# Optimization experiments

Hardware: AMD Instinct MI355X
Metric: run time of the kernel (lower is better)

Reference implementation:

```python
import jax, jax.numpy as jnp
import numpy as np

F_DIM = 64
GRID_CYL = (512, 48)   # (grid0=azimuth, grid1=z)
CYL_RANGE = (-3.14159265, -2.0, 3.14159265, 4.0)
CYL_VS = ((CYL_RANGE[2] - CYL_RANGE[0]) / GRID_CYL[0], (CYL_RANGE[3] - CYL_RANGE[1]) / GRID_CYL[1])
PC_RANGE = (0.0, -40.0, -3.0, 70.4, 40.0, 1.0)
BEV_VS = (0.32, 0.32)
GRID_BEV = (220, 250)  # (grid0=x, grid1=y)
BEV_SCALE_XY = GRID_BEV[0] * GRID_BEV[1]
BEV_SCALE_Y = GRID_BEV[1]
CYL_SCALE_XY = GRID_CYL[0] * GRID_CYL[1]
CYL_SCALE_Y = GRID_CYL[1]
BN_EPS = 1e-3


def _bn_relu(x, g, b):
    # train-mode BatchNorm1d over point axis; x: [N, C]
    m = x.mean(0)
    v = jnp.mean((x - m) ** 2, 0)
    return jax.nn.relu((x - m) * jax.lax.rsqrt(v + BN_EPS) * g + b)


def setup_inputs():
    rng = np.random.default_rng(0)
    B, NP = 4, 50000
    N = B * NP
    bidx = np.repeat(np.arange(B), NP).astype(np.float32)
    x = rng.uniform(0.5, 70.0, N).astype(np.float32)
    y = rng.uniform(-39.9, 39.9, N).astype(np.float32)
    z = rng.uniform(-2.9, 0.9, N).astype(np.float32)
    inten = rng.uniform(0.0, 1.0, N).astype(np.float32)
    points = np.stack([bidx, x, y, z, inten], 1)
    rho = np.sqrt(x * x + y * y)
    phi = np.arctan2(y, x)
    points_cyl = np.stack([phi, z, rho], 1).astype(np.float32)
    cyl_idxs = np.stack([(phi - CYL_RANGE[0]) / CYL_VS[0], (z - CYL_RANGE[1]) / CYL_VS[1]], 1)
    cyl_idxs = np.minimum(np.maximum(cyl_idxs, 0.0), np.array(GRID_CYL) - 1e-3).astype(np.float32)
    bev_idxs = np.stack([(x - PC_RANGE[0]) / BEV_VS[0], (y - PC_RANGE[1]) / BEV_VS[1]], 1)
    bev_idxs = np.minimum(np.maximum(bev_idxs, 0.0), np.array(GRID_BEV) - 1e-3).astype(np.float32)
    bev_merge = bidx.astype(np.int64) * BEV_SCALE_XY + np.floor(bev_idxs[:, 0]).astype(np.int64) * BEV_SCALE_Y + np.floor(bev_idxs[:, 1]).astype(np.int64)
    bev_unq, bev_inv = np.unique(bev_merge, return_inverse=True)
    cyl_merge = bidx.astype(np.int64) * CYL_SCALE_XY + np.floor(cyl_idxs[:, 0]).astype(np.int64) * CYL_SCALE_Y + np.floor(cyl_idxs[:, 1]).astype(np.int64)
    cyl_unq, cyl_inv = np.unique(cyl_merge, return_inverse=True)

    def lin(o, i):
        return (rng.standard_normal((o, i)) / np.sqrt(i)).astype(np.float32)

    w1 = lin(F_DIM, 16)
    w2 = lin(2 * F_DIM, F_DIM)
    w3 = lin(F_DIM, 2 * F_DIM)
    wc = (rng.standard_normal((F_DIM, F_DIM, 3, 3)) / np.sqrt(F_DIM * 9)).astype(np.float32)

    def bn(c):
        return (1.0 + 0.1 * rng.standard_normal(c)).astype(np.float32), (0.1 * rng.standard_normal(c)).astype(np.float32)

    g1, b1 = bn(F_DIM)
    g2, b2 = bn(2 * F_DIM)
    gc, bc = bn(F_DIM)
    g3, b3 = bn(F_DIM)
    return {
        'points': jnp.asarray(points), 'points_cyl': jnp.asarray(points_cyl),
        'cyl_idxs': jnp.asarray(cyl_idxs), 'bev_idxs': jnp.asarray(bev_idxs),
        'w1': jnp.asarray(w1), 'g1': jnp.asarray(g1), 'b1': jnp.asarray(b1),
        'w2': jnp.asarray(w2), 'g2': jnp.asarray(g2), 'b2': jnp.asarray(b2),
        'wc': jnp.asarray(wc), 'gc': jnp.asarray(gc), 'bc': jnp.asarray(bc),
        'w3': jnp.asarray(w3), 'g3': jnp.asarray(g3), 'b3': jnp.asarray(b3),
        'bev_unq_inv': jnp.asarray(bev_inv.astype(np.int32)),
        'bev_unq_coords': jnp.asarray(bev_unq.astype(np.int32)),
        'cyl_unq_inv': jnp.asarray(cyl_inv.astype(np.int32)),
        'cyl_unq_coords': jnp.asarray(cyl_unq.astype(np.int32)),
        'batch_size': B,
    }


def reference(points, points_cyl, cyl_idxs, bev_idxs, w1, g1, b1, w2, g2, b2, wc, gc, bc, w3, g3, b3, bev_unq_inv, bev_unq_coords, cyl_unq_inv, cyl_unq_coords, batch_size):
    N = points.shape[0]
    xyz = points[:, 1:4]
    feat = points[:, 4:]
    pbatch = points[:, 0].astype(jnp.int32)
    bev_c = jnp.floor(bev_idxs)
    cyl_c = jnp.floor(cyl_idxs)
    Nb = bev_unq_coords.shape[0]
    Nc = cyl_unq_coords.shape[0]
    ones = jnp.ones((N,), points.dtype)
    # scatter_mean + gather centering / clustering features
    cnt_b = jax.ops.segment_sum(ones, bev_unq_inv, Nb)
    bev_mean = jax.ops.segment_sum(xyz, bev_unq_inv, Nb) / cnt_b[:, None]
    bev_f_cluster = (xyz - bev_mean[bev_unq_inv])[:, :2]
    bev_f_center = xyz[:, :2] - ((bev_c + 0.5) * jnp.array(BEV_VS, points.dtype) + jnp.array(PC_RANGE[:2], points.dtype))
    cnt_c = jax.ops.segment_sum(ones, cyl_unq_inv, Nc)
    cyl_mean = jax.ops.segment_sum(points_cyl, cyl_unq_inv, Nc) / cnt_c[:, None]
    cyl_f_cluster = (points_cyl - cyl_mean[cyl_unq_inv])[:, :2]
    cyl_f_center = points_cyl[:, :2] - ((cyl_c + 0.5) * jnp.array(CYL_VS, points.dtype) + jnp.array(CYL_RANGE[:2], points.dtype))
    dist = jnp.sqrt(jnp.sum(xyz ** 2, 1, keepdims=True))
    mvf_in = jnp.concatenate([xyz, points_cyl, bev_f_center, cyl_f_center, bev_f_cluster, cyl_f_cluster, dist, feat], 1)  # [N,16]
    # input_transform: two 1x1 Conv1d (= matmul) + BN + ReLU
    h = _bn_relu(mvf_in @ w1.T, g1, b1)   # [N,64]
    h2 = _bn_relu(h @ w2.T, g2, b2)       # [N,128]
    pt_fea_cyl, pointwise = h2[:, :F_DIM], h2[:, F_DIM:]
    # cyl scatter_max -> dense range-view grid
    cyl_max = jax.ops.segment_max(pt_fea_cyl, cyl_unq_inv, Nc)  # [Nc,64]
    cb = cyl_unq_coords // CYL_SCALE_XY
    rem = cyl_unq_coords % CYL_SCALE_XY
    cx = rem // CYL_SCALE_Y
    cy = rem % CYL_SCALE_Y
    dense = jnp.zeros((batch_size, CYL_SCALE_XY, F_DIM), cyl_max.dtype)
    dense = dense.at[cb, cy * GRID_CYL[0] + cx].set(cyl_max)
    img = dense.reshape(batch_size, GRID_CYL[1], GRID_CYL[0], F_DIM).transpose(0, 3, 2, 1)  # NCHW, H=grid0, W=grid1
    # cyl_net proxy: Conv2d 3x3 + BN + ReLU
    img = jax.lax.conv_general_dilated(img, wc, (1, 1), 'SAME', dimension_numbers=('NCHW', 'OIHW', 'NCHW'))
    m = img.mean((0, 2, 3), keepdims=True)
    v = jnp.mean((img - m) ** 2, (0, 2, 3), keepdims=True)
    img = jax.nn.relu((img - m) * jax.lax.rsqrt(v + BN_EPS) * gc[None, :, None, None] + bc[None, :, None, None])
    im = img.transpose(0, 2, 3, 1)  # [B, grid0, grid1, F]
    # bilinear interpolation of per-point cyl features
    yq, xq = cyl_idxs[:, 0], cyl_idxs[:, 1]
    x0 = jnp.clip(jnp.floor(xq).astype(jnp.int32), 0, GRID_CYL[1] - 1)
    x1 = jnp.clip(jnp.floor(xq).astype(jnp.int32) + 1, 0, GRID_CYL[1] - 1)
    y0 = jnp.clip(jnp.floor(yq).astype(jnp.int32), 0, GRID_CYL[0] - 1)
    y1 = jnp.clip(jnp.floor(yq).astype(jnp.int32) + 1, 0, GRID_CYL[0] - 1)
    Ia = im[pbatch, y0, x0]
    Ib = im[pbatch, y1, x0]
    Ic = im[pbatch, y0, x1]
    Id = im[pbatch, y1, x1]
    x0f, x1f = x0.astype(xq.dtype), x1.astype(xq.dtype)
    y0f, y1f = y0.astype(yq.dtype), y1.astype(yq.dtype)
    wa = (x1f - xq) * (y1f - yq)
    wb_ = (x1f - xq) * (yq - y0f)
    wc_ = (xq - x0f) * (y1f - yq)
    wd = (xq - x0f) * (yq - y0f)
    point_cyl = Ia * wa[:, None] + Ib * wb_[:, None] + Ic * wc_[:, None] + Id * wd[:, None]  # [N,64]
    # mvf pointnet + bev scatter_max
    mvf2 = jnp.concatenate([pointwise, point_cyl], 1)  # [N,128]
    mvf_fea = _bn_relu(mvf2 @ w3.T, g3, b3)            # [N,64]
    bev_max = jax.ops.segment_max(mvf_fea, bev_unq_inv, Nb)  # [Nb,64] pillar features
    vb = bev_unq_coords // BEV_SCALE_XY
    vx = (bev_unq_coords % BEV_SCALE_XY) // BEV_SCALE_Y
    vy = bev_unq_coords % BEV_SCALE_Y
    voxel_coords = jnp.stack([vb, jnp.zeros_like(vb), vy, vx], 1)
    return mvf_fea, bev_max, voxel_coords
```

## Files before the change

kernel.cpp:

```cpp
#include <hip/hip_runtime.h>
#include <math.h>

#define BN_EPS 1e-3f

static constexpr float CR0 = -3.14159265f;
static constexpr float CR1 = -2.0f;
static constexpr float CVS0 = (float)((3.14159265 * 2.0) / 512.0);
static constexpr float CVS1 = (float)(6.0 / 48.0);
#define BEV_SXY (220 * 250)
#define BEV_SY 250

typedef __attribute__((ext_vector_type(8))) __bf16 bf16x8_t;
typedef __attribute__((ext_vector_type(4))) float f32x4_t;

union ABu { uint4 q; unsigned short us[8]; bf16x8_t bf; };

__device__ __forceinline__ float bnr(float x, float a, float b) {
    float v = fmaf(x, a, b);
    return v > 0.f ? v : 0.f;
}
__device__ __forceinline__ float bf2f(unsigned short u) {
    return __uint_as_float(((unsigned)u) << 16);
}
__device__ __forceinline__ unsigned short f2bf(float f) {
    unsigned u = __float_as_uint(f);
    u += 0x7FFFu + ((u >> 16) & 1u);
    return (unsigned short)(u >> 16);
}
__device__ __forceinline__ void bn_ab8(const float* stR, const float* g, const float* b,
                                       int C, int ch, float invn, float& a, float& bb) {
    float sm = 0.f, sq = 0.f;
#pragma unroll
    for (int r = 0; r < 8; r++) {
        sm += stR[r * 2 * C + ch];
        sq += stR[r * 2 * C + C + ch];
    }
    float m = sm * invn;
    float var = sq * invn - m * m;
    a = g[ch] * rsqrtf(var + BN_EPS);
    bb = b[ch] - m * a;
}

__device__ __forceinline__ unsigned fkey(float f) {
    unsigned u = __float_as_uint(f);
    return (u & 0x80000000u) ? ~u : (u | 0x80000000u);
}
__device__ __forceinline__ float dec_key(unsigned k, float a, float b) {
    if (k == 0u) return 0.f;
    unsigned u = (k & 0x80000000u) ? (k ^ 0x80000000u) : ~k;
    float v = fmaf(__uint_as_float(u), a, b);
    return v > 0.f ? v : 0.f;
}

__global__ void k_scatter_sums(const float* __restrict__ pts, const float* __restrict__ pcyl,
                               const int* __restrict__ binv, const int* __restrict__ cinv,
                               const float* __restrict__ wc, unsigned short* __restrict__ wctb,
                               unsigned long long* __restrict__ bacc,
                               unsigned long long* __restrict__ cacc,
                               int N, int Nb, int Nc) {
    int p = blockIdx.x * blockDim.x + threadIdx.x;
    if (p < 9 * 4096) {
        int j = p & 7, oc = (p >> 3) & 63, quad = (p >> 9) & 3, kc = (p >> 11) & 1, tap = p >> 12;
        int ic = kc * 32 + quad * 8 + j;
        wctb[p] = f2bf(wc[((oc * 64 + ic) * 3 + tap / 3) * 3 + tap % 3]);
    }
    if (p >= N) return;
    float x = pts[p * 5 + 1], y = pts[p * 5 + 2];
    float ph = pcyl[p * 3 + 0], z = pcyl[p * 3 + 1];
    int bi = binv[p], ci = cinv[p];
    unsigned long long xa = (1ull << 44) + (unsigned long long)(x * 1048576.0f + 0.5f);
    unsigned long long ya = (unsigned long long)((y + 40.0f) * 16777216.0f + 0.5f);
    unsigned long long pa = (1ull << 44) + (unsigned long long)((ph + 3.14159265f) * 16777216.0f + 0.5f);
    unsigned long long za = (unsigned long long)((z + 3.0f) * 16777216.0f + 0.5f);
    atomicAdd(&bacc[2 * (long)bi], xa);
    atomicAdd(&bacc[2 * (long)bi + 1], ya);
    atomicAdd(&cacc[2 * (long)ci], pa);
    atomicAdd(&cacc[2 * (long)ci + 1], za);
}

__global__ __launch_bounds__(256) void k_feat_gemm1(const float* __restrict__ pts,
        const float* __restrict__ pcyl, const float* __restrict__ cylidx,
        const float* __restrict__ bevidx, const int* __restrict__ binv,
        const int* __restrict__ cinv, const unsigned long long* __restrict__ bacc,
        const unsigned long long* __restrict__ cacc, const float* __restrict__ w1,
        unsigned short* __restrict__ h1b, float* __restrict__ st1o,
        int N, int Nb, int Nc) {
    __shared__ float w1s[1024];
    __shared__ unsigned int tbuf[32 * 260];
    int t = threadIdx.x;
    for (int i = t; i < 1024; i += 256) w1s[i] = w1[i];
    __syncthreads();
    int p = blockIdx.x * 256 + t;
    int pc = min(p, N - 1);
    float x = pts[pc * 5 + 1], y = pts[pc * 5 + 2], z = pts[pc * 5 + 3], inten = pts[pc * 5 + 4];
    float ph = pcyl[pc * 3 + 0], zc = pcyl[pc * 3 + 1], rho = pcyl[pc * 3 + 2];
    float ci0 = cylidx[pc * 2 + 0], ci1 = cylidx[pc * 2 + 1];
    float bi0 = bevidx[pc * 2 + 0], bi1 = bevidx[pc * 2 + 1];
    float bc0 = floorf(bi0), bc1 = floorf(bi1);
    float cc0 = floorf(ci0), cc1 = floorf(ci1);
    int bv = binv[pc], cv = cinv[pc];
    const unsigned long long MASK44 = (1ull << 44) - 1ull;
    unsigned long long A = bacc[2 * (long)bv], Bq = bacc[2 * (long)bv + 1];
    float bcnt = (float)(A >> 44);
    float rb = 1.0f / bcnt;
    float bmx = (float)(A & MASK44) * (1.0f / 1048576.0f) * rb;
    float bmy = (float)Bq * (1.0f / 16777216.0f) * rb - 40.0f;
    unsigned long long Cq = cacc[2 * (long)cv], Dq = cacc[2 * (long)cv + 1];
    float ccnt = (float)(Cq >> 44);
    float rc = 1.0f / ccnt;
    float cmp = (float)(Cq & MASK44) * (1.0f / 16777216.0f) * rc - 3.14159265f;
    float cmz = (float)Dq * (1.0f / 16777216.0f) * rc - 3.0f;
    float f[16];
    f[0] = x; f[1] = y; f[2] = z;
    f[3] = ph; f[4] = zc; f[5] = rho;
    f[6] = x - ((bc0 + 0.5f) * 0.32f + 0.0f);
    f[7] = y - ((bc1 + 0.5f) * 0.32f + (-40.0f));
    f[8] = ph - ((cc0 + 0.5f) * CVS0 + CR0);
    f[9] = zc - ((cc1 + 0.5f) * CVS1 + CR1);
    f[10] = x - bmx; f[11] = y - bmy;
    f[12] = ph - cmp; f[13] = zc - cmz;
    f[14] = sqrtf(x * x + y * y + z * z);
    f[15] = inten;
    for (int c2 = 0; c2 < 32; c2++) {
        float s0 = 0.f, s1 = 0.f;
        const float* w0 = &w1s[(2 * c2) * 16];
        const float* w1p = &w1s[(2 * c2 + 1) * 16];
#pragma unroll
        for (int k = 0; k < 16; k++) {
            s0 = fmaf(f[k], w0[k], s0);
            s1 = fmaf(f[k], w1p[k], s1);
        }
        tbuf[c2 * 260 + t] = (unsigned)f2bf(s0) | ((unsigned)f2bf(s1) << 16);
    }
    __syncthreads();
#pragma unroll
    for (int r = 0; r < 4; r++) {
        int cid = t + 256 * r;
        int pp = cid >> 2;
        int gp = blockIdx.x * 256 + pp;
        if (gp < N) {
            int c2b = (cid & 3) * 8;
            uint4 A2, Bv;
            A2.x = tbuf[(c2b + 0) * 260 + pp];
            A2.y = tbuf[(c2b + 1) * 260 + pp];
            A2.z = tbuf[(c2b + 2) * 260 + pp];
            A2.w = tbuf[(c2b + 3) * 260 + pp];
            Bv.x = tbuf[(c2b + 4) * 260 + pp];
            Bv.y = tbuf[(c2b + 5) * 260 + pp];
            Bv.z = tbuf[(c2b + 6) * 260 + pp];
            Bv.w = tbuf[(c2b + 7) * 260 + pp];
            uint4* dst = (uint4*)(h1b + (long)gp * 64 + (cid & 3) * 16);
            dst[0] = A2;
            dst[1] = Bv;
        }
    }
    {
        int ch = t & 63, grp = t >> 6;
        int c2 = ch >> 1, sh = (ch & 1) << 4;
        int nval = min(256, N - blockIdx.x * 256);
        float ss = 0.f, qq = 0.f;
        for (int i = 0; i < 64; i++) {
            int pp = grp * 64 + i;
            if (pp < nval) {
                unsigned uw = tbuf[c2 * 260 + pp];
                float v = bf2f((unsigned short)(uw >> sh));
                ss += v;
                qq = fmaf(v, v, qq);
            }
        }
        __syncthreads();
        w1s[t] = ss;
        w1s[256 + t] = qq;
        __syncthreads();
        if (t < 64) {
            float S = w1s[t] + w1s[64 + t] + w1s[128 + t] + w1s[192 + t];
            float Q = w1s[256 + t] + w1s[320 + t] + w1s[384 + t] + w1s[448 + t];
            float* dst = st1o + (blockIdx.x & 7) * 128;
            atomicAdd(&dst[t], S);
            atomicAdd(&dst[64 + t], Q);
        }
    }
}

__global__ __launch_bounds__(256, 2) void k_gemm2_mfma(const unsigned short* __restrict__ h1b,
        const float* __restrict__ w2, const float* __restrict__ st1R,
        const float* __restrict__ g1, const float* __restrict__ b1g, float invn,
        const float* __restrict__ pts, const float* __restrict__ cylidx,
        const float* __restrict__ g2full, unsigned int* __restrict__ gridk,
        unsigned short* __restrict__ h2b, float* __restrict__ st2o, int N) {
    __shared__ float redS[4][128], redQ[4][128];
    int t = threadIdx.x;
    int lane = t & 63;
    int c = lane & 15, quad = lane >> 4;
    int wv = t >> 6;
    int wid = (blockIdx.x * 256 + t) >> 6;
    int nw = gridDim.x * 4;
    bf16x8_t Bf[8][2];
#pragma unroll
    for (int tt = 0; tt < 8; tt++)
#pragma unroll
        for (int kc = 0; kc < 2; kc++) {
            const float* wr = w2 + (tt * 16 + c) * 64 + kc * 32 + quad * 8;
            float4 w0 = *(const float4*)wr;
            float4 w1 = *(const float4*)(wr + 4);
            ABu tmp;
            tmp.us[0] = f2bf(w0.x); tmp.us[1] = f2bf(w0.y);
            tmp.us[2] = f2bf(w0.z); tmp.us[3] = f2bf(w0.w);
            tmp.us[4] = f2bf(w1.x); tmp.us[5] = f2bf(w1.y);
            tmp.us[6] = f2bf(w1.z); tmp.us[7] = f2bf(w1.w);
            Bf[tt][kc] = tmp.bf;
        }
    float a1[16], b1[16];
#pragma unroll
    for (int kc = 0; kc < 2; kc++)
#pragma unroll
        for (int j = 0; j < 8; j++) {
            int ch = kc * 32 + quad * 8 + j;
            bn_ab8(st1R, g1, b1g, 64, ch, invn, a1[kc * 8 + j], b1[kc * 8 + j]);
        }
    unsigned sx[4];
#pragma unroll
    for (int tt = 0; tt < 4; tt++)
        sx[tt] = (g2full[tt * 16 + c] < 0.f) ? 0x80000000u : 0u;
    float s8[8], q8[8];
#pragma unroll
    for (int tt = 0; tt < 8; tt++) { s8[tt] = 0.f; q8[tt] = 0.f; }
    int ntiles = (N + 15) >> 4;
    for (int tile = wid; tile < ntiles; tile += nw) {
        int p0 = tile * 16;
        int pa = min(p0 + c, N - 1);
        int bsc = (int)pts[pa * 5];
        int ccx = (int)floorf(cylidx[pa * 2]);
        int ccy = (int)floorf(cylidx[pa * 2 + 1]);
        int cellbase = (((bsc * 512 + ccx) * 48) + ccy) * 64;
        bf16x8_t Af[2];
#pragma unroll
        for (int kc = 0; kc < 2; kc++) {
            ABu u;
            u.q = *(const uint4*)(h1b + (long)pa * 64 + kc * 32 + quad * 8);
            ABu o;
#pragma unroll
            for (int j = 0; j < 8; j++)
                o.us[j] = f2bf(bnr(bf2f(u.us[j]), a1[kc * 8 + j], b1[kc * 8 + j]));
            Af[kc] = o.bf;
        }
        f32x4_t acc[8];
#pragma unroll
        for (int tt = 0; tt < 8; tt++) acc[tt] = (f32x4_t){0.f, 0.f, 0.f, 0.f};
#pragma unroll
        for (int tt = 0; tt < 8; tt++) {
            acc[tt] = __builtin_amdgcn_mfma_f32_16x16x32_bf16(Af[0], Bf[tt][0], acc[tt], 0, 0, 0);
            acc[tt] = __builtin_amdgcn_mfma_f32_16x16x32_bf16(Af[1], Bf[tt][1], acc[tt], 0, 0, 0);
        }
#pragma unroll
        for (int r = 0; r < 4; r++) {
            int cb_r = __shfl(cellbase, quad * 4 + r);
            int pr = p0 + quad * 4 + r;
            bool ok = pr < N;
#pragma unroll
            for (int tt = 0; tt < 8; tt++) {
                unsigned short hv = f2bf(acc[tt][r]);
                if (ok) {
                    float xr = bf2f(hv);
                    s8[tt] += xr;
                    q8[tt] = fmaf(xr, xr, q8[tt]);
                    if (tt < 4) {
                        unsigned key = fkey(__uint_as_float(__float_as_uint(xr) ^ sx[tt]));
                        atomicMax(&gridk[cb_r + tt * 16 + c], key);
                    } else {
                        h2b[(long)pr * 64 + (tt - 4) * 16 + c] = hv;
                    }
                }
            }
        }
    }
#pragma unroll
    for (int tt = 0; tt < 8; tt++) {
        float ss = s8[tt], qq = q8[tt];
        ss += __shfl_xor(ss, 16); ss += __shfl_xor(ss, 32);
        qq += __shfl_xor(qq, 16); qq += __shfl_xor(qq, 32);
        if (quad == 0) { redS[wv][tt * 16 + c] = ss; redQ[wv][tt * 16 + c] = qq; }
    }
    __syncthreads();
    if (t < 128) {
        float S = redS[0][t] + redS[1][t] + redS[2][t] + redS[3][t];
        float Q = redQ[0][t] + redQ[1][t] + redQ[2][t] + redQ[3][t];
        float* dst = st2o + (blockIdx.x & 7) * 256;
        atomicAdd(&dst[t], S);
        atomicAdd(&dst[128 + t], Q);
    }
}

__global__ __launch_bounds__(768) void k_conv_lds(const unsigned int* __restrict__ gridk,
        const unsigned short* __restrict__ wctb, unsigned short* __restrict__ cb,
        const float* __restrict__ st2R, const float* __restrict__ g2,
        const float* __restrict__ b2g, float invn, float* __restrict__ stCo) {
    __shared__ unsigned short in_s[4 * 50 * 64];
    __shared__ unsigned short ob_s[2 * 48 * 64];
    __shared__ float as_[64], bs_[64];
    __shared__ float cS[12][16], cQ[12][16];
    int t = threadIdx.x;
    int lane = t & 63, wv = t >> 6;
    int n = lane & 15, quad = lane >> 4;
    int seg = wv >> 2, tt = wv & 3;
    int blk = blockIdx.x;
    int b = blk >> 8, r0 = (blk & 255) * 2;
    if (t < 64) {
        float av, bv;
        bn_ab8(st2R, g2, b2g, 128, t, invn, av, bv);
        as_[t] = fabsf(av);
        bs_[t] = bv;
    }
    bf16x8_t Bf[9][2];
    const unsigned short* wb = wctb + quad * 512 + (tt * 16 + n) * 8;
#pragma unroll
    for (int tap = 0; tap < 9; tap++)
#pragma unroll
        for (int kc = 0; kc < 2; kc++) {
            ABu u;
            u.q = *(const uint4*)(wb + (tap * 2 + kc) * 2048);
            Bf[tap][kc] = u.bf;
        }
    __syncthreads();
    for (int c = t; c < 1600; c += 768) {
        int row4 = c / 400;
        int rem = c % 400;
        int px = rem >> 3, ch8 = rem & 7;
        int gr = r0 + row4 - 1, gw = px - 1;
        ABu o;
        if (gr >= 0 && gr < 512 && gw >= 0 && gw < 48) {
            const unsigned int* src = gridk + (((long)b * 512 + gr) * 48 + gw) * 64 + ch8 * 8;
            uint4 k0 = *(const uint4*)src;
            uint4 k1 = *(const uint4*)(src + 4);
            const float* ap = &as_[ch8 * 8];
            const float* bp = &bs_[ch8 * 8];
            o.us[0] = f2bf(dec_key(k0.x, ap[0], bp[0]));
            o.us[1] = f2bf(dec_key(k0.y, ap[1], bp[1]));
            o.us[2] = f2bf(dec_key(k0.z, ap[2], bp[2]));
            o.us[3] = f2bf(dec_key(k0.w, ap[3], bp[3]));
            o.us[4] = f2bf(dec_key(k1.x, ap[4], bp[4]));
            o.us[5] = f2bf(dec_key(k1.y, ap[5], bp[5]));
            o.us[6] = f2bf(dec_key(k1.z, ap[6], bp[6]));
            o.us[7] = f2bf(dec_key(k1.w, ap[7], bp[7]));
        } else {
            o.q = make_uint4(0, 0, 0, 0);
        }
        *(uint4*)&in_s[(row4 * 50 + px) * 64 + ((ch8 ^ (px & 7)) << 3)] = o.q;
    }
    __syncthreads();
    float sC = 0.f, qC = 0.f;
    for (int rr = 0; rr < 2; rr++) {
        f32x4_t acc0 = (f32x4_t){0.f, 0.f, 0.f, 0.f};
        f32x4_t acc1 = (f32x4_t){0.f, 0.f, 0.f, 0.f};
#pragma unroll
        for (int tap = 0; tap < 9; tap++) {
            int row4 = tap / 3 + rr;
            int lpx = seg * 16 + n + tap % 3;
            const unsigned short* base = &in_s[(row4 * 50 + lpx) * 64];
            ABu a0, a1;
            a0.q = *(const uint4*)(base + ((quad ^ (lpx & 7)) << 3));
            a1.q = *(const uint4*)(base + (((4 + quad) ^ (lpx & 7)) << 3));
            acc0 = __builtin_amdgcn_mfma_f32_16x16x32_bf16(a0.bf, Bf[tap][0], acc0, 0, 0, 0);
            acc1 = __builtin_amdgcn_mfma_f32_16x16x32_bf16(a1.bf, Bf[tap][1], acc1, 0, 0, 0);
        }
#pragma unroll
        for (int r2 = 0; r2 < 4; r2++) {
            int px = seg * 16 + quad * 4 + r2;
            unsigned short hv = f2bf(acc0[r2] + acc1[r2]);
            ob_s[(rr * 48 + px) * 64 + tt * 16 + n] = hv;
            float xr = bf2f(hv);
            sC += xr;
            qC = fmaf(xr, xr, qC);
        }
    }
    sC += __shfl_xor(sC, 16); sC += __shfl_xor(sC, 32);
    qC += __shfl_xor(qC, 16); qC += __shfl_xor(qC, 32);
    if (quad == 0) { cS[wv][n] = sC; cQ[wv][n] = qC; }
    __syncthreads();
    if (t < 64) {
        int tt_ = t >> 4, n_ = t & 15;
        float S = cS[tt_][n_] + cS[tt_ + 4][n_] + cS[tt_ + 8][n_];
        float Q = cQ[tt_][n_] + cQ[tt_ + 4][n_] + cQ[tt_ + 8][n_];
        float* dst = stCo + (blockIdx.x & 7) * 128;
        atomicAdd(&dst[t], S);
        atomicAdd(&dst[64 + t], Q);
    }
    unsigned short* dst = cb + ((long)b * 512 + r0) * 48 * 64;
    *(uint4*)(dst + t * 8) = *(const uint4*)(ob_s + t * 8);
}

__global__ __launch_bounds__(256, 2) void k_gather3_mfma(const unsigned short* __restrict__ h2b,
        const unsigned short* __restrict__ convb, const float* __restrict__ st2R,
        const float* __restrict__ g2, const float* __restrict__ b2g,
        const float* __restrict__ stCR, const float* __restrict__ gc,
        const float* __restrict__ bcg, float invn, float invnC,
        const float* __restrict__ cylidx, const float* __restrict__ pts,
        const float* __restrict__ w3, unsigned short* __restrict__ h3b,
        float* __restrict__ st3o, int N) {
    __shared__ float rS[4][64], rQ[4][64];
    int t = threadIdx.x;
    int lane = t & 63;
    int c = lane & 15, quad = lane >> 4;
    int wv = t >> 6;
    int wid = (blockIdx.x * 256 + t) >> 6;
    int nw = gridDim.x * 4;
    bf16x8_t Bf[4][4];
#pragma unroll
    for (int tt = 0; tt < 4; tt++)
#pragma unroll
        for (int kc = 0; kc < 4; kc++) {
            const float* wr = w3 + (tt * 16 + c) * 128 + kc * 32 + quad * 8;
            float4 w0 = *(const float4*)wr;
            float4 w1 = *(const float4*)(wr + 4);
            ABu tmp;
            tmp.us[0] = f2bf(w0.x); tmp.us[1] = f2bf(w0.y);
            tmp.us[2] = f2bf(w0.z); tmp.us[3] = f2bf(w0.w);
            tmp.us[4] = f2bf(w1.x); tmp.us[5] = f2bf(w1.y);
            tmp.us[6] = f2bf(w1.z); tmp.us[7] = f2bf(w1.w);
            Bf[tt][kc] = tmp.bf;
        }
    float a2[16], b2[16], aC[16], bC[16];
#pragma unroll
    for (int kc = 0; kc < 2; kc++)
#pragma unroll
        for (int j = 0; j < 8; j++) {
            int kk = kc * 32 + quad * 8 + j;
            bn_ab8(st2R, g2, b2g, 128, 64 + kk, invn, a2[kc * 8 + j], b2[kc * 8 + j]);
            bn_ab8(stCR, gc, bcg, 64, kk, invnC, aC[kc * 8 + j], bC[kc * 8 + j]);
        }
    float s4[4], q4[4];
#pragma unroll
    for (int tt = 0; tt < 4; tt++) { s4[tt] = 0.f; q4[tt] = 0.f; }
    int ntiles = (N + 15) >> 4;
    for (int tile = wid; tile < ntiles; tile += nw) {
        int p0 = tile * 16;
        int p = min(p0 + c, N - 1);
        float yq = cylidx[p * 2], xq = cylidx[p * 2 + 1];
        int b = (int)pts[p * 5];
        int xf = (int)floorf(xq), yf = (int)floorf(yq);
        int x0 = min(max(xf, 0), 47);
        int x1 = min(max(xf + 1, 0), 47);
        int y0 = min(max(yf, 0), 511);
        int y1 = min(max(yf + 1, 0), 511);
        float x0f = (float)x0, x1f = (float)x1, y0f = (float)y0, y1f = (float)y1;
        float wa = (x1f - xq) * (y1f - yq);
        float wb = (x1f - xq) * (yq - y0f);
        float wc2 = (xq - x0f) * (y1f - yq);
        float wd = (xq - x0f) * (yq - y0f);
        const unsigned short* Ia = convb + (((long)b * 512 + y0) * 48 + x0) * 64;
        const unsigned short* Ib = convb + (((long)b * 512 + y1) * 48 + x0) * 64;
        const unsigned short* Ic = convb + (((long)b * 512 + y0) * 48 + x1) * 64;
        const unsigned short* Id = convb + (((long)b * 512 + y1) * 48 + x1) * 64;
        bf16x8_t Af[4];
#pragma unroll
        for (int kc = 0; kc < 2; kc++) {
            ABu u;
            u.q = *(const uint4*)(h2b + (long)p * 64 + kc * 32 + quad * 8);
            ABu o;
#pragma unroll
            for (int j = 0; j < 8; j++)
                o.us[j] = f2bf(bnr(bf2f(u.us[j]), a2[kc * 8 + j], b2[kc * 8 + j]));
            Af[kc] = o.bf;
        }
#pragma unroll
        for (int kc = 0; kc < 2; kc++) {
            int cbo = kc * 32 + quad * 8;
            ABu ua, ub, uc, ud;
            ua.q = *(const uint4*)(Ia + cbo);
            ub.q = *(const uint4*)(Ib + cbo);
            uc.q = *(const uint4*)(Ic + cbo);
            ud.q = *(const uint4*)(Id + cbo);
            ABu o;
#pragma unroll
            for (int j = 0; j < 8; j++) {
                float aa = aC[kc * 8 + j], bbv = bC[kc * 8 + j];
                float v = wa * bnr(bf2f(ua.us[j]), aa, bbv) + wb * bnr(bf2f(ub.us[j]), aa, bbv)
                        + wc2 * bnr(bf2f(uc.us[j]), aa, bbv) + wd * bnr(bf2f(ud.us[j]), aa, bbv);
                o.us[j] = f2bf(v);
            }
            Af[2 + kc] = o.bf;
        }
        f32x4_t acc[4];
#pragma unroll
        for (int tt = 0; tt < 4; tt++) acc[tt] = (f32x4_t){0.f, 0.f, 0.f, 0.f};
#pragma unroll
        for (int tt = 0; tt < 4; tt++)
#pragma unroll
            for (int kc = 0; kc < 4; kc++)
                acc[tt] = __builtin_amdgcn_mfma_f32_16x16x32_bf16(Af[kc], Bf[tt][kc], acc[tt], 0, 0, 0);
#pragma unroll
        for (int tt = 0; tt < 4; tt++)
#pragma unroll
            for (int r = 0; r < 4; r++) {
                int pr = p0 + quad * 4 + r;
                if (pr < N) {
                    unsigned short hv = f2bf(acc[tt][r]);
                    h3b[(long)pr * 64 + tt * 16 + c] = hv;
                    float xr = bf2f(hv);
                    s4[tt] += xr;
                    q4[tt] = fmaf(xr, xr, q4[tt]);
                }
            }
    }
#pragma unroll
    for (int tt = 0; tt < 4; tt++) {
        float ss = s4[tt], qq = q4[tt];
        ss += __shfl_xor(ss, 16); ss += __shfl_xor(ss, 32);
        qq += __shfl_xor(qq, 16); qq += __shfl_xor(qq, 32);
        if (quad == 0) { rS[wv][tt * 16 + c] = ss; rQ[wv][tt * 16 + c] = qq; }
    }
    __syncthreads();
    if (t < 64) {
        float S = rS[0][t] + rS[1][t] + rS[2][t] + rS[3][t];
        float Q = rQ[0][t] + rQ[1][t] + rQ[2][t] + rQ[3][t];
        float* dst = st3o + (blockIdx.x & 7) * 128;
        atomicAdd(&dst[t], S);
        atomicAdd(&dst[64 + t], Q);
    }
}

__global__ __launch_bounds__(256) void k_out_tile3(const unsigned short* __restrict__ h3b,
        const float* __restrict__ st3R, const float* __restrict__ g3,
        const float* __restrict__ b3g, float invn, const int* __restrict__ binv,
        float* __restrict__ out_fea, unsigned int* __restrict__ out_bev,
        const int* __restrict__ bcoords, float* __restrict__ out_vc, int Nb, int N) {
    int t = threadIdx.x, lane = t & 63, w = t >> 6;
    long gid = (long)blockIdx.x * 256 + t;
    if (gid < Nb) {
        int cc = bcoords[gid];
        int vb = cc / BEV_SXY;
        int rem = cc % BEV_SXY;
        int vx = rem / BEV_SY;
        int vy = rem % BEV_SY;
        out_vc[gid * 4 + 0] = (float)vb;
        out_vc[gid * 4 + 1] = 0.f;
        out_vc[gid * 4 + 2] = (float)vy;
        out_vc[gid * 4 + 3] = (float)vx;
    }
    int p = blockIdx.x * 4 + w;
    if (p >= N) return;
    float a, bb;
    bn_ab8(st3R, g3, b3g, 64, lane, invn, a, bb);
    float v = bnr(bf2f(h3b[(long)p * 64 + lane]), a, bb);
    out_fea[(long)p * 64 + lane] = v;
    int bi = binv[p];
    if (v > 0.f) {
        unsigned uv = __float_as_uint(v);
        unsigned* cell = out_bev + (long)bi * 64;
        unsigned cur = cell[lane];
        if (uv > cur) atomicMax(&cell[lane], uv);
    }
}

extern "C" void kernel_launch(void* const* d_in, const int* in_sizes, int n_in,
                              void* d_out, int out_size, void* d_ws, size_t ws_size,
                              hipStream_t stream) {
    const float* pts = (const float*)d_in[0];
    const float* pcyl = (const float*)d_in[1];
    const float* cylidx = (const float*)d_in[2];
    const float* bevidx = (const float*)d_in[3];
    const float* w1 = (const float*)d_in[4];
    const float* g1 = (const float*)d_in[5];
    const float* b1 = (const float*)d_in[6];
    const float* w2 = (const float*)d_in[7];
    const float* g2 = (const float*)d_in[8];
    const float* b2 = (const float*)d_in[9];
    const float* wc = (const float*)d_in[10];
    const float* gc = (const float*)d_in[11];
    const float* bc = (const float*)d_in[12];
    const float* w3 = (const float*)d_in[13];
    const float* g3 = (const float*)d_in[14];
    const float* b3 = (const float*)d_in[15];
    const int* binv = (const int*)d_in[16];
    const int* bcoords = (const int*)d_in[17];
    const int* cinv = (const int*)d_in[18];
    const int* ccoords = (const int*)d_in[19];
    int N = in_sizes[0] / 5;
    int Nb = in_sizes[17];
    int Nc = in_sizes[19];
    const int B = 4;
    const long GRIDSZ = (long)B * 512 * 48 * 64;
    float invN = 1.0f / (float)N;
    float invC = 1.0f / (float)(B * 512 * 48);

    char* wsb = (char*)d_ws;
    unsigned short* wctb = (unsigned short*)wsb;
    unsigned short* h2b = (unsigned short*)(wsb + 73728);
    unsigned short* h13b = (unsigned short*)(wsb + 73728 + 128L * N);
    unsigned int* gridk = (unsigned int*)(wsb + 73728 + 256L * N);
    unsigned long long* bacc = (unsigned long long*)(gridk + GRIDSZ);
    unsigned long long* cacc = bacc + 2L * Nb;
    float* stats = (float*)(cacc + 2L * Nc);
    float* st1R = stats;
    float* st2R = stats + 1024;
    float* st3R = stats + 3072;
    float* stCR = stats + 4096;
    unsigned short* convb = (unsigned short*)(stats + 5120);

    float* out_fea = (float*)d_out;
    unsigned int* out_bev = (unsigned int*)((float*)d_out + (long)N * 64);
    float* out_vc = (float*)d_out + (long)N * 64 + (long)Nb * 64;

    size_t zbytes = (size_t)GRIDSZ * 4 + (size_t)(2L * Nb + 2L * Nc) * 8 + 5120 * 4;
    hipMemsetAsync(gridk, 0, zbytes, stream);
    hipMemsetAsync(out_bev, 0, (size_t)Nb * 64 * 4, stream);

    int nb256 = (N + 255) / 256;
    k_scatter_sums<<<nb256, 256, 0, stream>>>(pts, pcyl, binv, cinv, wc, wctb, bacc, cacc, N, Nb, Nc);
    k_feat_gemm1<<<nb256, 256, 0, stream>>>(pts, pcyl, cylidx, bevidx, binv, cinv, bacc, cacc, w1, h13b, st1R, N, Nb, Nc);
    k_gemm2_mfma<<<512, 256, 0, stream>>>(h13b, w2, st1R, g1, b1, invN, pts, cylidx, g2, gridk, h2b, st2R, N);
    k_conv_lds<<<1024, 768, 0, stream>>>(gridk, wctb, convb, st2R, g2, b2, invN, stCR);
    k_gather3_mfma<<<512, 256, 0, stream>>>(h2b, convb, st2R, g2, b2, stCR, gc, bc, invN, invC, cylidx, pts, w3, h13b, st3R, N);
    k_out_tile3<<<(N + 3) / 4, 256, 0, stream>>>(h13b, st3R, g3, b3, invN, binv, out_fea, out_bev, bcoords, out_vc, Nb, N);
}
```

Measured before the change: 368.4 us.

## Fuse BEV scatter-max into gather3 via pre-BN monotone keys, decode later

Moves the BEV segment-max out of the final elementwise kernel and into the GEMM3 kernel. There it atomically maxes an order-preserving key of the pre-BatchNorm value, sign-flipped by gamma so the order matches the post-BN value. The final kernel then decodes each pillar cell by applying the BN affine and ReLU. This drops the binv read and the conditional atomics from the output pass. In exchange it issues an unconditional atomic for every point and channel inside the MFMA kernel, which may contend more, and it relies on fkey/dec_key helpers that must already exist.

```diff
diff --git a/kernel.cpp b/kernel.cpp
--- a/kernel.cpp
+++ b/kernel.cpp
@@ -395,8 +395,9 @@
         const float* __restrict__ stCR, const float* __restrict__ gc,
         const float* __restrict__ bcg, float invn, float invnC,
         const float* __restrict__ cylidx, const float* __restrict__ pts,
-        const float* __restrict__ w3, unsigned short* __restrict__ h3b,
-        float* __restrict__ st3o, int N) {
+        const float* __restrict__ w3, const int* __restrict__ binv,
+        const float* __restrict__ g3full, unsigned int* __restrict__ bevk,
+        unsigned short* __restrict__ h3b, float* __restrict__ st3o, int N) {
     __shared__ float rS[4][64], rQ[4][64];
     int t = threadIdx.x;
     int lane = t & 63;
@@ -428,6 +429,10 @@
             bn_ab8(st2R, g2, b2g, 128, 64 + kk, invn, a2[kc * 8 + j], b2[kc * 8 + j]);
             bn_ab8(stCR, gc, bcg, 64, kk, invnC, aC[kc * 8 + j], bC[kc * 8 + j]);
         }
+    unsigned sx3[4];
+#pragma unroll
+    for (int tt = 0; tt < 4; tt++)
+        sx3[tt] = (g3full[tt * 16 + c] < 0.f) ? 0x80000000u : 0u;
     float s4[4], q4[4];
 #pragma unroll
     for (int tt = 0; tt < 4; tt++) { s4[tt] = 0.f; q4[tt] = 0.f; }
@@ -437,6 +442,7 @@
         int p = min(p0 + c, N - 1);
         float yq = cylidx[p * 2], xq = cylidx[p * 2 + 1];
         int b = (int)pts[p * 5];
+        int bevc = binv[p] * 64;
         int xf = (int)floorf(xq), yf = (int)floorf(yq);
         int x0 = min(max(xf, 0), 47);
         int x1 = min(max(xf + 1, 0), 47);
@@ -489,18 +495,23 @@
             for (int kc = 0; kc < 4; kc++)
                 acc[tt] = __builtin_amdgcn_mfma_f32_16x16x32_bf16(Af[kc], Bf[tt][kc], acc[tt], 0, 0, 0);
 #pragma unroll
-        for (int tt = 0; tt < 4; tt++)
-#pragma unroll
-            for (int r = 0; r < 4; r++) {
-                int pr = p0 + quad * 4 + r;
-                if (pr < N) {
-                    unsigned short hv = f2bf(acc[tt][r]);
+        for (int r = 0; r < 4; r++) {
+            int cb_r = __shfl(bevc, quad * 4 + r);
+            int pr = p0 + quad * 4 + r;
+            bool ok = pr < N;
+#pragma unroll
+            for (int tt = 0; tt < 4; tt++) {
+                unsigned short hv = f2bf(acc[tt][r]);
+                if (ok) {
                     h3b[(long)pr * 64 + tt * 16 + c] = hv;
                     float xr = bf2f(hv);
                     s4[tt] += xr;
                     q4[tt] = fmaf(xr, xr, q4[tt]);
+                    unsigned key = fkey(__uint_as_float(__float_as_uint(xr) ^ sx3[tt]));
+                    atomicMax(&bevk[cb_r + tt * 16 + c], key);
                 }
             }
+        }
     }
 #pragma unroll
     for (int tt = 0; tt < 4; tt++) {
@@ -521,7 +532,7 @@
 
 __global__ __launch_bounds__(256) void k_out_tile3(const unsigned short* __restrict__ h3b,
         const float* __restrict__ st3R, const float* __restrict__ g3,
-        const float* __restrict__ b3g, float invn, const int* __restrict__ binv,
+        const float* __restrict__ b3g, float invn,
         float* __restrict__ out_fea, unsigned int* __restrict__ out_bev,
         const int* __restrict__ bcoords, float* __restrict__ out_vc, int Nb, int N) {
     int t = threadIdx.x, lane = t & 63, w = t >> 6;
@@ -537,19 +548,20 @@
         out_vc[gid * 4 + 2] = (float)vy;
         out_vc[gid * 4 + 3] = (float)vx;
     }
+    if (gid < (long)Nb * 64) {
+        int ch = (int)(gid & 63);
+        float a, bb;
+        bn_ab8(st3R, g3, b3g, 64, ch, invn, a, bb);
+        unsigned k = out_bev[gid];
+        float v = dec_key(k, fabsf(a), bb);
+        out_bev[gid] = __float_as_uint(v);
+    }
     int p = blockIdx.x * 4 + w;
     if (p >= N) return;
     float a, bb;
     bn_ab8(st3R, g3, b3g, 64, lane, invn, a, bb);
     float v = bnr(bf2f(h3b[(long)p * 64 + lane]), a, bb);
     out_fea[(long)p * 64 + lane] = v;
-    int bi = binv[p];
-    if (v > 0.f) {
-        unsigned uv = __float_as_uint(v);
-        unsigned* cell = out_bev + (long)bi * 64;
-        unsigned cur = cell[lane];
-        if (uv > cur) atomicMax(&cell[lane], uv);
-    }
 }
 
 extern "C" void kernel_launch(void* const* d_in, const int* in_sizes, int n_in,
@@ -610,6 +622,6 @@
     k_feat_gemm1<<<nb256, 256, 0, stream>>>(pts, pcyl, cylidx, bevidx, binv, cinv, bacc, cacc, w1, h13b, st1R, N, Nb, Nc);
     k_gemm2_mfma<<<512, 256, 0, stream>>>(h13b, w2, st1R, g1, b1, invN, pts, cylidx, g2, gridk, h2b, st2R, N);
     k_conv_lds<<<1024, 768, 0, stream>>>(gridk, wctb, convb, st2R, g2, b2, invN, stCR);
-    k_gather3_mfma<<<512, 256, 0, stream>>>(h2b, convb, st2R, g2, b2, stCR, gc, bc, invN, invC, cylidx, pts, w3, h13b, st3R, N);
-    k_out_tile3<<<(N + 3) / 4, 256, 0, stream>>>(h13b, st3R, g3, b3, invN, binv, out_fea, out_bev, bcoords, out_vc, Nb, N);
-}
+    k_gather3_mfma<<<512, 256, 0, stream>>>(h2b, convb, st2R, g2, b2, stCR, gc, bc, invN, invC, cylidx, pts, w3, binv, g3, out_bev, h13b, st3R, N);
+    k_out_tile3<<<(N + 3) / 4, 256, 0, stream>>>(h13b, st3R, g3, b3, invN, out_fea, out_bev, bcoords, out_vc, Nb, N);
+}
```

After: 387.3 us. 5.1% more time.
